# Kernel optimization log

Measured on AMD Instinct MI355X. Metric: run time of the kernel, lower is better.

The kernel has to match this reference:

```python
import math
import jax, jax.numpy as jnp
import numpy as np

E = 1024          # n_embd
H = 16            # n_head
KVH = 8           # n_kv_head
N_REP = H // KVH  # 2
HD = E // H // 2  # 32, differential attention halves head_dim
DEPTH = 12
LAMBDA_INIT = 0.8 - 0.6 * math.exp(-0.3 * DEPTH)
EPS = 1e-6
ROPE_BASE = 10000.0


def rope_tables(T):
    inv_freq = 1.0 / (ROPE_BASE ** (np.arange(0, HD, 2, dtype=np.float32) / HD))
    t = np.arange(T, dtype=np.float32)
    freqs = np.outer(t, inv_freq)  # [T, HD/2]
    return jnp.asarray(np.cos(freqs)), jnp.asarray(np.sin(freqs))


def apply_rope(x, cos, sin):
    # x: [B, T, nH, HD]; cos/sin: [T, HD/2] broadcast to [1,T,1,HD/2]
    d = x.shape[-1] // 2
    c = cos[None, :, None, :]
    s = sin[None, :, None, :]
    x1, x2 = x[..., :d], x[..., d:]
    return jnp.concatenate([x1 * c + x2 * s, -x1 * s + x2 * c], axis=-1)


def causal_attn(q, k, v, scale):
    # q: [B,T,H,HD], k: [B,T,H,HD], v: [B,T,H,Dv] -> [B,T,H,Dv]
    T = q.shape[1]
    mask = jnp.tril(jnp.ones((T, T), dtype=bool))
    s = jnp.einsum('bthd,bshd->bhts', q, k) * scale
    s = jnp.where(mask[None, None], s, jnp.finfo(s.dtype).min)
    p = jax.nn.softmax(s, axis=-1)
    return jnp.einsum('bhts,bshd->bthd', p, v)


def setup_inputs() -> dict:
    key = jax.random.key(0)
    ks = jax.random.split(key, 10)
    s = 0.02
    return {
        'x': jax.random.normal(ks[0], (4, 1024, E), jnp.float32),
        'Wq': jax.random.normal(ks[1], (E, E), jnp.float32) * s,
        'Wk': jax.random.normal(ks[2], (E, E // N_REP), jnp.float32) * s,
        'Wv': jax.random.normal(ks[3], (E, E // N_REP), jnp.float32) * s,
        'Wo': jax.random.normal(ks[4], (E, E), jnp.float32) * s,
        'lambda_q1': jax.random.normal(ks[5], (HD,), jnp.float32) * 0.1,
        'lambda_k1': jax.random.normal(ks[6], (HD,), jnp.float32) * 0.1,
        'lambda_q2': jax.random.normal(ks[7], (HD,), jnp.float32) * 0.1,
        'lambda_k2': jax.random.normal(ks[8], (HD,), jnp.float32) * 0.1,
        'rms_w': jnp.ones((2 * HD,), jnp.float32),
    }


def reference(x, Wq, Wk, Wv, Wo, lambda_q1, lambda_k1, lambda_q2, lambda_k2, rms_w):
    B, T, _ = x.shape
    q = (x @ Wq).reshape(B, T, 2 * H, HD)
    k = (x @ Wk).reshape(B, T, 2 * KVH, HD)
    v = (x @ Wv).reshape(B, T, KVH, 2, HD)

    cos, sin = rope_tables(T)
    q = apply_rope(q, cos, sin)
    k = apply_rope(k, cos, sin)

    q = q.reshape(B, T, H, 2, HD)
    k = k.reshape(B, T, KVH, 2, HD)
    q1, q2 = q[:, :, :, 0], q[:, :, :, 1]
    k1, k2 = k[:, :, :, 0], k[:, :, :, 1]
    # concat v1||v2 so each softmax is computed once against 2*HD-wide V
    vcat = v.reshape(B, T, KVH, 2 * HD)

    # GQA: repeat kv heads to match query heads
    k1 = jnp.repeat(k1, N_REP, axis=2)
    k2 = jnp.repeat(k2, N_REP, axis=2)
    vcat = jnp.repeat(vcat, N_REP, axis=2)

    scale = HD ** -0.5  # flash_attn default softmax scale
    attn1 = causal_attn(q1, k1, vcat, scale)  # [B,T,H,2*HD] = cat(attn11, attn12)
    attn2 = causal_attn(q2, k2, vcat, scale)  # [B,T,H,2*HD] = cat(attn21, attn22)

    lambda_1 = jnp.exp(jnp.sum(lambda_q1 * lambda_k1))
    lambda_2 = jnp.exp(jnp.sum(lambda_q2 * lambda_k2))
    lambda_full = lambda_1 - lambda_2 + LAMBDA_INIT

    attn = attn1 - lambda_full * attn2
    # RMSNorm over last dim (2*HD)
    rms = jnp.sqrt(jnp.mean(attn * attn, axis=-1, keepdims=True) + EPS)
    attn = (attn / rms) * rms_w
    attn = attn * (1.0 - LAMBDA_INIT)

    attn = attn.reshape(B, T, H * 2 * HD)
    return attn @ Wo
```

## Files before the change

### kernel.cpp

```cpp
#include <hip/hip_runtime.h>

typedef unsigned short u16;
typedef unsigned int   u32;
typedef __attribute__((ext_vector_type(8))) short short8;
typedef __attribute__((ext_vector_type(4))) float f32x4;
typedef __attribute__((ext_vector_type(16))) float f32x16;
typedef __attribute__((ext_vector_type(4))) u32 u32x4;
typedef __attribute__((ext_vector_type(2))) u32 u32x2;

#define LAMBDA_INIT_F 0.78360576653162444f
#define SCALE_QK      0.17677669529663687f


__device__ __forceinline__ u16 f2bf(float f) {
  u32 u = __float_as_uint(f);
  u32 r = (u + 0x7fffu + ((u >> 16) & 1u)) >> 16;
  return (u16)r;
}
__device__ __forceinline__ float bf2f(u16 h) {
  return __uint_as_float(((u32)h) << 16);
}
__device__ __forceinline__ void gload_lds16(const u16* g, u16* l) {
  __builtin_amdgcn_global_load_lds((const __attribute__((address_space(1))) u32*)g,
                                   (__attribute__((address_space(3))) u32*)l, 16, 0, 0);
}


__global__ void k_cvt_x(const float* __restrict__ x, u16* __restrict__ xb) {
  int id = blockIdx.x * 256 + threadIdx.x;
  float4 v = ((const float4*)x)[id];
  u16* o = xb + (size_t)id * 4;
  o[0] = f2bf(v.x); o[1] = f2bf(v.y); o[2] = f2bf(v.z); o[3] = f2bf(v.w);
}

__global__ void k_transpose(const float* __restrict__ Wq, const float* __restrict__ Wk,
                            const float* __restrict__ Wv, const float* __restrict__ Wo,
                            u16* __restrict__ wt, u16* __restrict__ wot) {
  __shared__ float tile[32][33];
  const float* src; u16* dst; int N;
  switch (blockIdx.z) {
    case 0: src = Wq; dst = wt;               N = 1024; break;
    case 1: src = Wk; dst = wt + 1024 * 1024; N = 512;  break;
    case 2: src = Wv; dst = wt + 1536 * 1024; N = 512;  break;
    default: src = Wo; dst = wot;             N = 1024; break;
  }
  int nb = blockIdx.x * 32, kb = blockIdx.y * 32;
  if (nb >= N) return;
  int tx = threadIdx.x, ty = threadIdx.y;
  #pragma unroll
  for (int i = 0; i < 32; i += 8)
    tile[ty + i][tx] = src[(size_t)(kb + ty + i) * N + nb + tx];
  __syncthreads();
  #pragma unroll
  for (int i = 0; i < 32; i += 8)
    dst[(size_t)(nb + ty + i) * 1024 + kb + tx] = f2bf(tile[tx][ty + i]);
}

__global__ void k_rope_tab(float* __restrict__ cosT, float* __restrict__ sinT) {
  int id = blockIdx.x * 256 + threadIdx.x;
  if (id >= 16384) return;
  int t = id >> 4, i = id & 15;
  float inv = powf(10000.0f, -(float)i * (1.0f / 16.0f));
  float f = (float)t * inv;
  float sv, cv; sincosf(f, &sv, &cv);
  cosT[id] = cv; sinT[id] = sv;
}


__global__ __launch_bounds__(256) void gemm_bt(const u16* __restrict__ A, const u16* __restrict__ Bt,
                                               float* __restrict__ C, int M, int N, int K, int ldc) {
  __shared__ u16 As[128 * 32];
  __shared__ u16 Bs[128 * 32];
  const int tid = threadIdx.x;
  const int wid = tid >> 6, lane = tid & 63;
  const int m0 = blockIdx.y * 128, n0 = blockIdx.x * 128;
  const int wr = wid >> 1, wc = wid & 1;
  f32x4 acc[4][4];
  #pragma unroll
  for (int m = 0; m < 4; ++m)
    #pragma unroll
    for (int n = 0; n < 4; ++n) acc[m][n] = (f32x4){0.f, 0.f, 0.f, 0.f};
  const int lrow = lane >> 2;
  const int lcol = (lane & 3) * 8;
  for (int k0 = 0; k0 < K; k0 += 32) {
    #pragma unroll
    for (int i = 0; i < 2; ++i) {
      const int c = wid + i * 4;
      const int row = c * 16 + lrow;
      gload_lds16(A  + (size_t)(m0 + row) * K + k0 + lcol, &As[c * 512]);
      gload_lds16(Bt + (size_t)(n0 + row) * K + k0 + lcol, &Bs[c * 512]);
    }
    __syncthreads();
    const int fr = lane & 15, fc = (lane >> 4) * 8;
    short8 af[4], bfr[4];
    #pragma unroll
    for (int m = 0; m < 4; ++m) af[m]  = *(const short8*)&As[(wr * 64 + m * 16 + fr) * 32 + fc];
    #pragma unroll
    for (int n = 0; n < 4; ++n) bfr[n] = *(const short8*)&Bs[(wc * 64 + n * 16 + fr) * 32 + fc];
    #pragma unroll
    for (int m = 0; m < 4; ++m)
      #pragma unroll
      for (int n = 0; n < 4; ++n)
        acc[m][n] = __builtin_amdgcn_mfma_f32_16x16x32_bf16(af[m], bfr[n], acc[m][n], 0, 0, 0);
    __syncthreads();
  }
  const int fr = lane & 15, fg = lane >> 4;
  #pragma unroll
  for (int m = 0; m < 4; ++m)
    #pragma unroll
    for (int n = 0; n < 4; ++n)
      #pragma unroll
      for (int r = 0; r < 4; ++r) {
        const int row = m0 + wr * 64 + m * 16 + fg * 4 + r;
        const int col = n0 + wc * 64 + n * 16 + fr;
        C[(size_t)row * ldc + col] = acc[m][n][r];
      }
}


__global__ void k_rope_reorg(const float* __restrict__ qkv, const float* __restrict__ cosT,
                             const float* __restrict__ sinT,
                             u16* __restrict__ q1, u16* __restrict__ q2,
                             u16* __restrict__ k1, u16* __restrict__ k2) {
  int id = blockIdx.x * 256 + threadIdx.x;
  const int NQ = 4096 * 32 * 16;
  const int NK = 4096 * 16 * 16;
  if (id < NQ) {
    int m = id >> 9, r = id & 511;
    int qh = r >> 4, d = r & 15;
    int b = m >> 10, t = m & 1023;
    float x1 = qkv[(size_t)m * 2048 + qh * 32 + d];
    float x2 = qkv[(size_t)m * 2048 + qh * 32 + d + 16];
    float c = cosT[t * 16 + d], s = sinT[t * 16 + d];
    float o1 = (x1 * c + x2 * s) * SCALE_QK, o2 = (x2 * c - x1 * s) * SCALE_QK;
    int h = qh >> 1, comp = qh & 1;
    u16* dst = comp ? q2 : q1;
    size_t base = ((size_t)(b * 16 + h) * 1024 + t) * 32 + d;
    dst[base] = f2bf(o1); dst[base + 16] = f2bf(o2);
  } else if (id < NQ + NK) {
    int id2 = id - NQ;
    int m = id2 >> 8, r = id2 & 255;
    int kh = r >> 4, d = r & 15;
    int b = m >> 10, t = m & 1023;
    float x1 = qkv[(size_t)m * 2048 + 1024 + kh * 32 + d];
    float x2 = qkv[(size_t)m * 2048 + 1024 + kh * 32 + d + 16];
    float c = cosT[t * 16 + d], s = sinT[t * 16 + d];
    float o1 = x1 * c + x2 * s, o2 = x2 * c - x1 * s;
    int kvh = kh >> 1, comp = kh & 1;
    u16* dst = comp ? k2 : k1;
    size_t base = ((size_t)(b * 8 + kvh) * 1024 + t) * 32 + d;
    dst[base] = f2bf(o1); dst[base + 16] = f2bf(o2);
  }
}

__global__ void k_vt(const float* __restrict__ qkv, u16* __restrict__ vt) {
  __shared__ float tile[32][33];
  int bh = blockIdx.z;
  int b = bh >> 3, kvh = bh & 7;
  int t0 = blockIdx.x * 32, j0 = blockIdx.y * 32;
  int tx = threadIdx.x, ty = threadIdx.y;
  const float* src = qkv + (size_t)b * 1024 * 2048 + 1536 + kvh * 64;
  #pragma unroll
  for (int i = 0; i < 32; i += 8)
    tile[ty + i][tx] = src[(size_t)(t0 + ty + i) * 2048 + j0 + tx];
  __syncthreads();
  u16* dst = vt + ((size_t)bh * 64 + j0) * 1024 + t0;
  #pragma unroll
  for (int i = 0; i < 32; i += 8)
    dst[(size_t)(ty + i) * 1024 + tx] = f2bf(tile[tx][ty + i]);
}


#define KSTR 40
#define VSTR 88
#define PSTR 88

__global__ __launch_bounds__(256) void attn_mfma(
    const u16* __restrict__ q1g, const u16* __restrict__ q2g,
    const u16* __restrict__ k1g, const u16* __restrict__ k2g,
    const u16* __restrict__ vtg,
    float* __restrict__ a1, float* __restrict__ a2) {
  __shared__ u16 Kl[64 * KSTR];
  __shared__ u16 Vl[64 * VSTR];
  __shared__ u16 Pl[4 * 32 * PSTR];

  const int bid = blockIdx.x;
  const int qb = bid & 7, prob = bid >> 3;
  const int comp = prob & 1, h = (prob >> 1) & 15, b = prob >> 5;
  const int tid = threadIdx.x;
  const int w = tid >> 6, lane = tid & 63;
  const int hi = lane >> 5, c = lane & 31;

  const u16* Qc  = (comp ? q2g : q1g) + (size_t)(b * 16 + h) * 1024 * 32;
  const u16* Kc  = (comp ? k2g : k1g) + (size_t)(b * 8 + (h >> 1)) * 1024 * 32;
  const u16* Vtc = vtg + (size_t)(b * 8 + (h >> 1)) * 64 * 1024;

  const int qbase = qb * 128;
  const int q = qbase + w * 32 + c;
  const int qmaxw = qbase + w * 32 + 31;

  short8 qf0 = *(const short8*)&Qc[(size_t)q * 32 + hi * 8];
  short8 qf1 = *(const short8*)&Qc[(size_t)q * 32 + 16 + hi * 8];

  f32x16 acc0, acc1;
  #pragma unroll
  for (int r = 0; r < 16; ++r) { acc0[r] = 0.f; acc1[r] = 0.f; }
  float m_run = -1e30f, l_run = 0.f;

  const int ntiles = qb * 2 + 2;

  const int krow = tid >> 2, kseg = tid & 3;
  const int vrow = tid >> 3, vseg = tid & 7;
  u32x4 kr, vr0, vr1;
  kr  = *(const u32x4*)&Kc[(size_t)krow * 32 + kseg * 8];
  vr0 = *(const u32x4*)&Vtc[(size_t)vrow * 1024 + vseg * 8];
  vr1 = *(const u32x4*)&Vtc[(size_t)(vrow + 32) * 1024 + vseg * 8];

  for (int t = 0; t < ntiles; ++t) {
    const int kv0 = t * 64;
    __syncthreads();
    *(u32x4*)&Kl[krow * KSTR + kseg * 8] = kr;
    *(u32x4*)&Vl[vrow * VSTR + vseg * 8] = vr0;
    *(u32x4*)&Vl[(vrow + 32) * VSTR + vseg * 8] = vr1;
    __syncthreads();
    if (t + 1 < ntiles) {
      const int kn = kv0 + 64;
      kr  = *(const u32x4*)&Kc[(size_t)(kn + krow) * 32 + kseg * 8];
      vr0 = *(const u32x4*)&Vtc[(size_t)vrow * 1024 + kn + vseg * 8];
      vr1 = *(const u32x4*)&Vtc[(size_t)(vrow + 32) * 1024 + kn + vseg * 8];
    }
    if (kv0 > qmaxw) continue;

    f32x16 s0, s1;
    #pragma unroll
    for (int r = 0; r < 16; ++r) { s0[r] = 0.f; s1[r] = 0.f; }
    {
      short8 kf00 = *(const short8*)&Kl[c * KSTR + hi * 8];
      short8 kf01 = *(const short8*)&Kl[c * KSTR + 16 + hi * 8];
      short8 kf10 = *(const short8*)&Kl[(32 + c) * KSTR + hi * 8];
      short8 kf11 = *(const short8*)&Kl[(32 + c) * KSTR + 16 + hi * 8];
      s0 = __builtin_amdgcn_mfma_f32_32x32x16_bf16(kf00, qf0, s0, 0, 0, 0);
      s0 = __builtin_amdgcn_mfma_f32_32x32x16_bf16(kf01, qf1, s0, 0, 0, 0);
      s1 = __builtin_amdgcn_mfma_f32_32x32x16_bf16(kf10, qf0, s1, 0, 0, 0);
      s1 = __builtin_amdgcn_mfma_f32_32x32x16_bf16(kf11, qf1, s1, 0, 0, 0);
    }

    float sv[32];
    #pragma unroll
    for (int r = 0; r < 16; ++r) { sv[r] = s0[r]; sv[16 + r] = s1[r]; }

    if (kv0 + 63 > qbase + w * 32) {
      #pragma unroll
      for (int r = 0; r < 32; ++r) {
        int kv = kv0 + (r >> 4) * 32 + (r & 3) + 8 * ((r >> 2) & 3) + 4 * hi;
        if (kv > q) sv[r] = -1e30f;
      }
    }

    float mt = sv[0];
    #pragma unroll
    for (int r = 1; r < 32; ++r) mt = fmaxf(mt, sv[r]);
    mt = fmaxf(mt, __shfl_xor(mt, 32));
    float m_new = fmaxf(m_run, mt);
    float alpha = __expf(m_run - m_new);
    float tsum = 0.f;
    #pragma unroll
    for (int r = 0; r < 32; ++r) { sv[r] = __expf(sv[r] - m_new); tsum += sv[r]; }
    tsum += __shfl_xor(tsum, 32);
    l_run = l_run * alpha + tsum;
    m_run = m_new;
    #pragma unroll
    for (int r = 0; r < 16; ++r) { acc0[r] *= alpha; acc1[r] *= alpha; }

    u16* Pw = &Pl[(w * 32 + c) * PSTR];
    #pragma unroll
    for (int half = 0; half < 2; ++half)
      #pragma unroll
      for (int rr = 0; rr < 4; ++rr) {
        u32 u0 = __float_as_uint(sv[half * 16 + rr * 4 + 0]) + 0x8000u;
        u32 u1 = __float_as_uint(sv[half * 16 + rr * 4 + 1]) + 0x8000u;
        u32 u2 = __float_as_uint(sv[half * 16 + rr * 4 + 2]) + 0x8000u;
        u32 u3 = __float_as_uint(sv[half * 16 + rr * 4 + 3]) + 0x8000u;
        u32x2 wv;
        wv[0] = (u0 >> 16) | (u1 & 0xffff0000u);
        wv[1] = (u2 >> 16) | (u3 & 0xffff0000u);
        *(u32x2*)&Pw[half * 32 + rr * 8 + hi * 4] = wv;
      }

    const u16* Pr = &Pl[(w * 32 + c) * PSTR];
    #pragma unroll
    for (int kc = 0; kc < 4; ++kc) {
      short8 pf  = *(const short8*)&Pr[kc * 16 + hi * 8];
      short8 vf0 = *(const short8*)&Vl[c * VSTR + kc * 16 + hi * 8];
      short8 vf1 = *(const short8*)&Vl[(32 + c) * VSTR + kc * 16 + hi * 8];
      acc0 = __builtin_amdgcn_mfma_f32_32x32x16_bf16(vf0, pf, acc0, 0, 0, 0);
      acc1 = __builtin_amdgcn_mfma_f32_32x32x16_bf16(vf1, pf, acc1, 0, 0, 0);
    }
  }

  float inv = 1.f / l_run;
  float* ao = (comp ? a2 : a1) + ((size_t)(b * 1024 + q)) * 1024 + h * 64;
  #pragma unroll
  for (int rr = 0; rr < 4; ++rr) {
    float4 o0 = { acc0[rr * 4 + 0] * inv, acc0[rr * 4 + 1] * inv,
                  acc0[rr * 4 + 2] * inv, acc0[rr * 4 + 3] * inv };
    float4 o1 = { acc1[rr * 4 + 0] * inv, acc1[rr * 4 + 1] * inv,
                  acc1[rr * 4 + 2] * inv, acc1[rr * 4 + 3] * inv };
    *(float4*)&ao[rr * 8 + hi * 4] = o0;
    *(float4*)&ao[32 + rr * 8 + hi * 4] = o1;
  }
}


__global__ void k_diff_rms(const float* __restrict__ a1, const float* __restrict__ a2in,
                           const float* __restrict__ lq1, const float* __restrict__ lk1,
                           const float* __restrict__ lq2, const float* __restrict__ lk2,
                           const float* __restrict__ rmsw, u16* __restrict__ out) {
  int id = blockIdx.x * 256 + threadIdx.x;
  if (id >= 65536) return;
  float s1 = 0.f, s2 = 0.f;
  #pragma unroll
  for (int i = 0; i < 32; ++i) { s1 += lq1[i] * lk1[i]; s2 += lq2[i] * lk2[i]; }
  float lam = __expf(s1) - __expf(s2) + LAMBDA_INIT_F;
  const float* p1 = a1 + (size_t)id * 64;
  const float* p2 = a2in + (size_t)id * 64;
  float y[64]; float ss = 0.f;
  #pragma unroll
  for (int d = 0; d < 64; ++d) { float v = p1[d] - lam * p2[d]; y[d] = v; ss += v * v; }
  float inv = rsqrtf(ss * (1.f / 64.f) + 1e-6f) * (1.f - LAMBDA_INIT_F);
  u16* o = out + (size_t)id * 64;
  #pragma unroll
  for (int d = 0; d < 64; ++d) o[d] = f2bf(y[d] * inv * rmsw[d]);
}


extern "C" void kernel_launch(void* const* d_in, const int* in_sizes, int n_in,
                              void* d_out, int out_size, void* d_ws, size_t ws_size,
                              hipStream_t stream) {
  (void)in_sizes; (void)n_in; (void)out_size; (void)ws_size;
  const float* x    = (const float*)d_in[0];
  const float* Wq   = (const float*)d_in[1];
  const float* Wk   = (const float*)d_in[2];
  const float* Wv   = (const float*)d_in[3];
  const float* Wo   = (const float*)d_in[4];
  const float* lq1  = (const float*)d_in[5];
  const float* lk1  = (const float*)d_in[6];
  const float* lq2  = (const float*)d_in[7];
  const float* lk2  = (const float*)d_in[8];
  const float* rmsw = (const float*)d_in[9];
  float* out = (float*)d_out;

  char* ws = (char*)d_ws;
  size_t off = 0;
  auto alloc = [&](size_t bytes) { void* p = ws + off; off += (bytes + 255) & ~(size_t)255; return p; };
  u16*   xb   = (u16*)  alloc(4096ULL * 1024 * 2);
  u16*   wt   = (u16*)  alloc(2048ULL * 1024 * 2);
  u16*   wot  = (u16*)  alloc(1024ULL * 1024 * 2);
  float* qkv  = (float*)alloc(4096ULL * 2048 * 4);
  float* cosT = (float*)alloc(16384ULL * 4);
  float* sinT = (float*)alloc(16384ULL * 4);
  u16*   q1   = (u16*)  alloc(4ULL * 16 * 1024 * 32 * 2);
  u16*   q2   = (u16*)  alloc(4ULL * 16 * 1024 * 32 * 2);
  u16*   k1   = (u16*)  alloc(4ULL * 8 * 1024 * 32 * 2);
  u16*   k2   = (u16*)  alloc(4ULL * 8 * 1024 * 32 * 2);
  u16*   vt   = (u16*)  alloc(4ULL * 8 * 64 * 1024 * 2);
  float* a1   = (float*)alloc(4096ULL * 1024 * 4);
  float* a2   = (float*)alloc(4096ULL * 1024 * 4);
  u16*   am   = (u16*)  alloc(4096ULL * 1024 * 2);

  hipLaunchKernelGGL(k_cvt_x, dim3(4096), dim3(256), 0, stream, x, xb);
  hipLaunchKernelGGL(k_transpose, dim3(32, 32, 4), dim3(32, 8), 0, stream, Wq, Wk, Wv, Wo, wt, wot);
  hipLaunchKernelGGL(k_rope_tab, dim3(64), dim3(256), 0, stream, cosT, sinT);
  hipLaunchKernelGGL(gemm_bt, dim3(16, 32), dim3(256), 0, stream, xb, wt, qkv, 4096, 2048, 1024, 2048);
  hipLaunchKernelGGL(k_rope_reorg, dim3(12288), dim3(256), 0, stream, qkv, cosT, sinT, q1, q2, k1, k2);
  hipLaunchKernelGGL(k_vt, dim3(32, 2, 32), dim3(32, 8), 0, stream, qkv, vt);
  hipLaunchKernelGGL(attn_mfma, dim3(1024), dim3(256), 0, stream, q1, q2, k1, k2, vt, a1, a2);
  hipLaunchKernelGGL(k_diff_rms, dim3(256), dim3(256), 0, stream, a1, a2, lq1, lk1, lq2, lk2, rmsw, am);
  hipLaunchKernelGGL(gemm_bt, dim3(8, 32), dim3(256), 0, stream, am, wot, out, 4096, 1024, 1024, 1024);
}
```

Measured before the change: 231.8 us.

## Store QKV projection in bf16 and reorder attention blocks for causal balance

The QKV GEMM now writes bf16 output instead of fp32, and the rope/reorg and V-transpose kernels read bf16. This halves the intermediate QKV traffic (about 32MB down to 16MB) and drops one rounding step in the V transpose. Separately, the attention grid mapping interleaves heavy and light causal query blocks so that long- and short-running blocks are mixed across the launch, aiming for better load balance. Rounding Q/K to bf16 before RoPE adds a small precision change, since the values were later converted to bf16 anyway.

```diff
diff --git a/kernel.cpp b/kernel.cpp
--- a/kernel.cpp
+++ b/kernel.cpp
@@ -67,8 +67,9 @@
 }
 
 
+template<int OBF16>
 __global__ __launch_bounds__(256) void gemm_bt(const u16* __restrict__ A, const u16* __restrict__ Bt,
-                                               float* __restrict__ C, int M, int N, int K, int ldc) {
+                                               void* __restrict__ Cv, int M, int N, int K, int ldc) {
   __shared__ u16 As[128 * 32];
   __shared__ u16 Bs[128 * 32];
   const int tid = threadIdx.x;
@@ -85,10 +86,10 @@
   for (int k0 = 0; k0 < K; k0 += 32) {
     #pragma unroll
     for (int i = 0; i < 2; ++i) {
-      const int c = wid + i * 4;
-      const int row = c * 16 + lrow;
-      gload_lds16(A  + (size_t)(m0 + row) * K + k0 + lcol, &As[c * 512]);
-      gload_lds16(Bt + (size_t)(n0 + row) * K + k0 + lcol, &Bs[c * 512]);
+      const int ch = wid + i * 4;
+      const int row = ch * 16 + lrow;
+      gload_lds16(A  + (size_t)(m0 + row) * K + k0 + lcol, &As[ch * 512]);
+      gload_lds16(Bt + (size_t)(n0 + row) * K + k0 + lcol, &Bs[ch * 512]);
     }
     __syncthreads();
     const int fr = lane & 15, fc = (lane >> 4) * 8;
@@ -113,12 +114,13 @@
       for (int r = 0; r < 4; ++r) {
         const int row = m0 + wr * 64 + m * 16 + fg * 4 + r;
         const int col = n0 + wc * 64 + n * 16 + fr;
-        C[(size_t)row * ldc + col] = acc[m][n][r];
+        if (OBF16) ((u16*)Cv)[(size_t)row * ldc + col] = f2bf(acc[m][n][r]);
+        else       ((float*)Cv)[(size_t)row * ldc + col] = acc[m][n][r];
       }
 }
 
 
-__global__ void k_rope_reorg(const float* __restrict__ qkv, const float* __restrict__ cosT,
+__global__ void k_rope_reorg(const u16* __restrict__ qkvb, const float* __restrict__ cosT,
                              const float* __restrict__ sinT,
                              u16* __restrict__ q1, u16* __restrict__ q2,
                              u16* __restrict__ k1, u16* __restrict__ k2) {
@@ -129,8 +131,8 @@
     int m = id >> 9, r = id & 511;
     int qh = r >> 4, d = r & 15;
     int b = m >> 10, t = m & 1023;
-    float x1 = qkv[(size_t)m * 2048 + qh * 32 + d];
-    float x2 = qkv[(size_t)m * 2048 + qh * 32 + d + 16];
+    float x1 = bf2f(qkvb[(size_t)m * 2048 + qh * 32 + d]);
+    float x2 = bf2f(qkvb[(size_t)m * 2048 + qh * 32 + d + 16]);
     float c = cosT[t * 16 + d], s = sinT[t * 16 + d];
     float o1 = (x1 * c + x2 * s) * SCALE_QK, o2 = (x2 * c - x1 * s) * SCALE_QK;
     int h = qh >> 1, comp = qh & 1;
@@ -142,8 +144,8 @@
     int m = id2 >> 8, r = id2 & 255;
     int kh = r >> 4, d = r & 15;
     int b = m >> 10, t = m & 1023;
-    float x1 = qkv[(size_t)m * 2048 + 1024 + kh * 32 + d];
-    float x2 = qkv[(size_t)m * 2048 + 1024 + kh * 32 + d + 16];
+    float x1 = bf2f(qkvb[(size_t)m * 2048 + 1024 + kh * 32 + d]);
+    float x2 = bf2f(qkvb[(size_t)m * 2048 + 1024 + kh * 32 + d + 16]);
     float c = cosT[t * 16 + d], s = sinT[t * 16 + d];
     float o1 = x1 * c + x2 * s, o2 = x2 * c - x1 * s;
     int kvh = kh >> 1, comp = kh & 1;
@@ -153,13 +155,13 @@
   }
 }
 
-__global__ void k_vt(const float* __restrict__ qkv, u16* __restrict__ vt) {
-  __shared__ float tile[32][33];
+__global__ void k_vt(const u16* __restrict__ qkvb, u16* __restrict__ vt) {
+  __shared__ u16 tile[32][34];
   int bh = blockIdx.z;
   int b = bh >> 3, kvh = bh & 7;
   int t0 = blockIdx.x * 32, j0 = blockIdx.y * 32;
   int tx = threadIdx.x, ty = threadIdx.y;
-  const float* src = qkv + (size_t)b * 1024 * 2048 + 1536 + kvh * 64;
+  const u16* src = qkvb + (size_t)b * 1024 * 2048 + 1536 + kvh * 64;
   #pragma unroll
   for (int i = 0; i < 32; i += 8)
     tile[ty + i][tx] = src[(size_t)(t0 + ty + i) * 2048 + j0 + tx];
@@ -167,7 +169,7 @@
   u16* dst = vt + ((size_t)bh * 64 + j0) * 1024 + t0;
   #pragma unroll
   for (int i = 0; i < 32; i += 8)
-    dst[(size_t)(ty + i) * 1024 + tx] = f2bf(tile[tx][ty + i]);
+    dst[(size_t)(ty + i) * 1024 + tx] = tile[tx][ty + i];
 }
 
 
@@ -185,7 +187,9 @@
   __shared__ u16 Pl[4 * 32 * PSTR];
 
   const int bid = blockIdx.x;
-  const int qb = bid & 7, prob = bid >> 3;
+  const int y = bid & 7, xx = (bid >> 3) & 7, g = bid >> 6;
+  const int qb = (xx & 1) ? (xx >> 1) : (7 - (xx >> 1));
+  const int prob = g * 8 + y;
   const int comp = prob & 1, h = (prob >> 1) & 15, b = prob >> 5;
   const int tid = threadIdx.x;
   const int w = tid >> 6, lane = tid & 63;
@@ -353,28 +357,28 @@
   char* ws = (char*)d_ws;
   size_t off = 0;
   auto alloc = [&](size_t bytes) { void* p = ws + off; off += (bytes + 255) & ~(size_t)255; return p; };
-  u16*   xb   = (u16*)  alloc(4096ULL * 1024 * 2);
-  u16*   wt   = (u16*)  alloc(2048ULL * 1024 * 2);
-  u16*   wot  = (u16*)  alloc(1024ULL * 1024 * 2);
-  float* qkv  = (float*)alloc(4096ULL * 2048 * 4);
-  float* cosT = (float*)alloc(16384ULL * 4);
-  float* sinT = (float*)alloc(16384ULL * 4);
-  u16*   q1   = (u16*)  alloc(4ULL * 16 * 1024 * 32 * 2);
-  u16*   q2   = (u16*)  alloc(4ULL * 16 * 1024 * 32 * 2);
-  u16*   k1   = (u16*)  alloc(4ULL * 8 * 1024 * 32 * 2);
-  u16*   k2   = (u16*)  alloc(4ULL * 8 * 1024 * 32 * 2);
-  u16*   vt   = (u16*)  alloc(4ULL * 8 * 64 * 1024 * 2);
-  float* a1   = (float*)alloc(4096ULL * 1024 * 4);
-  float* a2   = (float*)alloc(4096ULL * 1024 * 4);
-  u16*   am   = (u16*)  alloc(4096ULL * 1024 * 2);
+  u16*   xb    = (u16*)  alloc(4096ULL * 1024 * 2);
+  u16*   wt    = (u16*)  alloc(2048ULL * 1024 * 2);
+  u16*   wot   = (u16*)  alloc(1024ULL * 1024 * 2);
+  u16*   qkvb  = (u16*)  alloc(4096ULL * 2048 * 2);
+  float* cosT  = (float*)alloc(16384ULL * 4);
+  float* sinT  = (float*)alloc(16384ULL * 4);
+  u16*   q1    = (u16*)  alloc(4ULL * 16 * 1024 * 32 * 2);
+  u16*   q2    = (u16*)  alloc(4ULL * 16 * 1024 * 32 * 2);
+  u16*   k1    = (u16*)  alloc(4ULL * 8 * 1024 * 32 * 2);
+  u16*   k2    = (u16*)  alloc(4ULL * 8 * 1024 * 32 * 2);
+  u16*   vt    = (u16*)  alloc(4ULL * 8 * 64 * 1024 * 2);
+  float* a1    = (float*)alloc(4096ULL * 1024 * 4);
+  float* a2    = (float*)alloc(4096ULL * 1024 * 4);
+  u16*   am    = (u16*)  alloc(4096ULL * 1024 * 2);
 
   hipLaunchKernelGGL(k_cvt_x, dim3(4096), dim3(256), 0, stream, x, xb);
   hipLaunchKernelGGL(k_transpose, dim3(32, 32, 4), dim3(32, 8), 0, stream, Wq, Wk, Wv, Wo, wt, wot);
   hipLaunchKernelGGL(k_rope_tab, dim3(64), dim3(256), 0, stream, cosT, sinT);
-  hipLaunchKernelGGL(gemm_bt, dim3(16, 32), dim3(256), 0, stream, xb, wt, qkv, 4096, 2048, 1024, 2048);
-  hipLaunchKernelGGL(k_rope_reorg, dim3(12288), dim3(256), 0, stream, qkv, cosT, sinT, q1, q2, k1, k2);
-  hipLaunchKernelGGL(k_vt, dim3(32, 2, 32), dim3(32, 8), 0, stream, qkv, vt);
+  hipLaunchKernelGGL((gemm_bt<1>), dim3(16, 32), dim3(256), 0, stream, xb, wt, (void*)qkvb, 4096, 2048, 1024, 2048);
+  hipLaunchKernelGGL(k_rope_reorg, dim3(12288), dim3(256), 0, stream, qkvb, cosT, sinT, q1, q2, k1, k2);
+  hipLaunchKernelGGL(k_vt, dim3(32, 2, 32), dim3(32, 8), 0, stream, qkvb, vt);
   hipLaunchKernelGGL(attn_mfma, dim3(1024), dim3(256), 0, stream, q1, q2, k1, k2, vt, a1, a2);
   hipLaunchKernelGGL(k_diff_rms, dim3(256), dim3(256), 0, stream, a1, a2, lq1, lk1, lq2, lk2, rmsw, am);
-  hipLaunchKernelGGL(gemm_bt, dim3(8, 32), dim3(256), 0, stream, am, wot, out, 4096, 1024, 1024, 1024);
-}
+  hipLaunchKernelGGL((gemm_bt<0>), dim3(8, 32), dim3(256), 0, stream, am, wot, (void*)out, 4096, 1024, 1024, 1024);
+}
```

After: 228.5 us. About the same (-1.4%).
